# Performance work log

Hardware: AMD Instinct MI355X
Metric: run time of the kernel (lower is better)

## Reference

```python
import jax, jax.numpy as jnp
import numpy as np

PATCH_ORIG = (5, 15, 15)
DWS = [(1, 4, 4), (1, 2, 2), (1, 1, 1)]
STRIDE = [(1, 6, 6), (1, 6, 6), (1, 3, 3)]
EMBED = 32
EPS = 1e-6


def _extract_full_patches(x, shape, stride):
    # x: (N,C,D,H,W) -> (N*P, C, *shape) patches (torch unfold + permute + view)
    N, C = x.shape[:2]
    sp = x.shape[2:]
    nb = tuple((sp[i] - shape[i]) // stride[i] + 1 for i in range(3))
    d = (jnp.arange(nb[0]) * stride[0])[:, None] + jnp.arange(shape[0])[None, :]
    h = (jnp.arange(nb[1]) * stride[1])[:, None] + jnp.arange(shape[1])[None, :]
    w = (jnp.arange(nb[2]) * stride[2])[:, None] + jnp.arange(shape[2])[None, :]
    pat = x[:, :, d[:, None, None, :, None, None],
                  h[None, :, None, None, :, None],
                  w[None, None, :, None, None, :]]
    # (N, C, nb0, nb1, nb2, p0, p1, p2) -> (N*P, C, p0, p1, p2)
    pat = pat.transpose(0, 2, 3, 4, 1, 5, 6, 7).reshape(-1, C, *shape)
    return pat, nb


def _extract_centers(x, stride, offset, nb):
    # 1x1x1 patches at fixed crop offset, limited to nb -> (N*P, C)
    sl = x[:, :, offset[0]::stride[0], offset[1]::stride[1], offset[2]::stride[2]]
    sl = sl[:, :, :nb[0], :nb[1], :nb[2]]
    N, C = sl.shape[:2]
    return sl.transpose(0, 2, 3, 4, 1).reshape(-1, C)


def _maxpool(x, fct):
    # MaxPool3d(kernel=stride=fct) on exactly-divisible dims via reshape trick
    B, C = x.shape[:2]
    p0, p1, p2 = x.shape[2] // fct[0], x.shape[3] // fct[1], x.shape[4] // fct[2]
    x = x.reshape(B, C, p0, fct[0], p1, fct[1], p2, fct[2])
    return x.max(axis=(3, 5, 7))


def _dice(pred, trg):
    # inferno SorensenDiceLoss, channelwise: flatten to (C, -1)
    p = pred.transpose(1, 0, 2, 3, 4).reshape(pred.shape[1], -1)
    t = trg.transpose(1, 0, 2, 3, 4).reshape(trg.shape[1], -1)
    num = (p * t).sum(-1)
    den = jnp.clip((p * p + t * t).sum(-1), EPS, None)
    return (-2.0 * num / den).sum()


def _level_loss(pred, target, W, b, lvl):
    gt = target[:, :1].astype(jnp.float32)           # GT label volume (N,1,D,H,W)
    affs = target[:, 1:].astype(jnp.float32)
    bnd = 1.0 - affs
    bmask = bnd[:, 4:].max(1, keepdims=True) if lvl == 0 else bnd[:, :4].max(1, keepdims=True)
    dws, stride = DWS[lvl], STRIDE[lvl]
    pshape = tuple(p * f for p, f in zip(PATCH_ORIG, dws))
    off = tuple(s // 2 for s in pshape)              # crop offset (rnd crop fixed to 0)

    gt_patches, nb = _extract_full_patches(gt, pshape, stride)   # (P,1,*pshape)
    centers = _extract_centers(gt, stride, off, nb)[:, 0]        # (P,)
    on_bnd = _extract_centers(bmask, stride, off, nb)[:, 0]      # (P,)

    me = (gt_patches != centers[:, None, None, None, None]).astype(jnp.float32)
    ign = (gt_patches == 0).astype(jnp.float32)
    valid = ((centers != 0) & (on_bnd != 1.0)).astype(jnp.float32)

    trg = _maxpool(me, dws)                                      # (P,1,*PATCH_ORIG)
    ign_m = _maxpool(ign, dws) > 0

    emb = _extract_centers(pred, stride, off, nb)                # (P, EMBED)
    pp = jax.nn.sigmoid(emb @ W + b).reshape(-1, 1, *PATCH_ORIG) # patch decoder

    pp = jnp.where(ign_m, 0.0, pp)
    trg = jnp.where(ign_m, 0.0, trg)
    v = valid[:, None, None, None, None]                         # mask == select valid patches for sum-based Dice
    return _dice(pp * v, trg * v)


def setup_inputs() -> dict:
    key = jax.random.key(0)
    ks = jax.random.split(key, 16)
    shapes = [(2, 8, 160, 160), (2, 8, 80, 80), (2, 8, 40, 40)]
    inp = {}
    for lvl, (n, d, hh, ww) in enumerate(shapes):
        inp[f'pred{lvl}'] = jax.random.normal(ks[lvl], (n, EMBED, d, hh, ww), jnp.float32)
        gt = jax.random.randint(ks[3 + lvl], (n, 1, d, hh, ww), 0, 50, jnp.int32)
        affs = jax.random.randint(ks[6 + lvl], (n, 8, d, hh, ww), 0, 2, jnp.int32)
        inp[f'tgt{lvl}'] = jnp.concatenate([gt, affs], axis=1)
        inp[f'W{lvl}'] = 0.1 * jax.random.normal(ks[9 + lvl], (EMBED, int(np.prod(PATCH_ORIG))), jnp.float32)
        inp[f'b{lvl}'] = jnp.zeros((int(np.prod(PATCH_ORIG)),), jnp.float32)
    return inp


def reference(pred0, pred1, pred2, W0, b0, W1, b1, W2, b2, tgt0, tgt1, tgt2):
    loss = _level_loss(pred0, tgt0, W0, b0, 0)
    loss = loss + _level_loss(pred1, tgt1, W1, b1, 1)
    loss = loss + _level_loss(pred2, tgt2, W2, b2, 2)
    return loss
```

## Files before the change

### kernel.cpp

```cpp
#include <hip/hip_runtime.h>
#include <hip/hip_bf16.h>


constexpr int NBATCH = 2;
constexpr int EMB = 32;
constexpr int TGTC = 9;
constexpr int PZ = 5, PY = 15, PX = 15;
constexpr int P = PZ * PY * PX;

constexpr int NBLK0 = NBATCH * 4 * 17 * 17;
constexpr int NBLK1 = NBATCH * 4 * 9 * 9;
constexpr int NBLK2 = NBATCH * 4 * 9 * 9;
constexpr int NBLK_TOT = NBLK0 + NBLK1 + NBLK2;

template <int D, int H, int W,
          int NB0, int NBH, int NBW,
          int SH, int SW,
          int DH, int DWIN,
          int OFFZ, int OFFY, int OFFX,
          int AFFB>
__device__ __forceinline__
void level_body(const int lbid,
                const float* __restrict__ pred,
                const int* __restrict__ tgt,
                const float* __restrict__ Wm,
                const float* __restrict__ bv,
                float* __restrict__ partials)
{
    const int tid = threadIdx.x;

    int k  = lbid % NBW;
    int t1 = lbid / NBW;
    int j  = t1 % NBH;
    int t2 = t1 / NBH;
    int i  = t2 % NB0;
    int b  = t2 / NB0;

    const int HW = H * W;
    const int CH = D * HW;
    const int zc = OFFZ + i;
    const int yc = OFFY + j * SH;
    const int xc = OFFX + k * SW;
    const int cidx = zc * HW + yc * W + xc;

    __shared__ float s_emb[EMB];
    __shared__ int   s_c;
    __shared__ int   s_valid;

    if (tid == 0) {
        const int c = tgt[b * TGTC * CH + cidx];
        bool allaff = true;
        #pragma unroll
        for (int ch = 0; ch < 4; ++ch)
            allaff &= (tgt[(b * TGTC + AFFB + ch) * CH + cidx] != 0);
        s_c = c;
        s_valid = (c != 0) && allaff;
    }
    __syncthreads();

    if (!s_valid) {
        if (tid == 0) {
            partials[2 * lbid]     = 0.0f;
            partials[2 * lbid + 1] = 0.0f;
        }
        return;
    }

    if (tid < EMB)
        s_emb[tid] = pred[(b * EMB + tid) * CH + cidx];
    __syncthreads();

    const int* __restrict__ gtb = tgt + b * TGTC * CH;
    const int c = s_c;

    float num = 0.0f, den = 0.0f;
    for (int o = tid; o < P; o += 256) {
        const int pz = o / (PY * PX);
        const int r  = o - pz * (PY * PX);
        const int py = r / PX;
        const int px = r - py * PX;

        float dot = bv[o];
        #pragma unroll
        for (int e = 0; e < EMB; ++e)
            dot = fmaf(s_emb[e], Wm[e * P + o], dot);
        float pp = 1.0f / (1.0f + expf(-dot));

        const int zb = i + pz;
        const int yb = j * SH + py * DH;
        const int xb = k * SW + px * DWIN;
        bool anyz = false, anyd = false;
        #pragma unroll
        for (int wy = 0; wy < DH; ++wy) {
            #pragma unroll
            for (int wx = 0; wx < DWIN; ++wx) {
                const int g = gtb[zb * HW + (yb + wy) * W + (xb + wx)];
                anyz |= (g == 0);
                anyd |= (g != c);
            }
        }
        float trg = (anyz || !anyd) ? 0.0f : 1.0f;
        if (anyz) pp = 0.0f;

        num = fmaf(pp, trg, num);
        den += pp * pp + trg * trg;
    }

    #pragma unroll
    for (int off = 32; off > 0; off >>= 1) {
        num += __shfl_down(num, off);
        den += __shfl_down(den, off);
    }
    __shared__ float sn[4], sd[4];
    if ((tid & 63) == 0) { sn[tid >> 6] = num; sd[tid >> 6] = den; }
    __syncthreads();
    if (tid == 0) {
        partials[2 * lbid]     = sn[0] + sn[1] + sn[2] + sn[3];
        partials[2 * lbid + 1] = sd[0] + sd[1] + sd[2] + sd[3];
    }
}

__global__ __launch_bounds__(256)
void stage_kernel(const float* __restrict__ pred0, const int* __restrict__ tgt0,
                  const float* __restrict__ W0, const float* __restrict__ b0,
                  const float* __restrict__ pred1, const int* __restrict__ tgt1,
                  const float* __restrict__ W1, const float* __restrict__ b1,
                  const float* __restrict__ pred2, const int* __restrict__ tgt2,
                  const float* __restrict__ W2, const float* __restrict__ b2,
                  float* __restrict__ partials)
{
    const int gb = blockIdx.x;
    if (gb < NBLK0) {
        level_body<8, 160, 160, 4, 17, 17, 6, 6, 4, 4, 2, 30, 30, 5>(
            gb, pred0, tgt0, W0, b0, partials);
    } else if (gb < NBLK0 + NBLK1) {
        level_body<8, 80, 80, 4, 9, 9, 6, 6, 2, 2, 2, 15, 15, 1>(
            gb - NBLK0, pred1, tgt1, W1, b1, partials + 2 * NBLK0);
    } else {
        level_body<8, 40, 40, 4, 9, 9, 3, 3, 1, 1, 2, 7, 7, 1>(
            gb - NBLK0 - NBLK1, pred2, tgt2, W2, b2,
            partials + 2 * (NBLK0 + NBLK1));
    }
}

__global__ __launch_bounds__(256)
void finalize_kernel(const float* __restrict__ partials, float* __restrict__ out)
{
    const int tid = threadIdx.x;
    const int counts[3] = { NBLK0, NBLK1, NBLK2 };
    const int offs[3]   = { 0, NBLK0, NBLK0 + NBLK1 };

    __shared__ float sn[4], sd[4];
    __shared__ float s_loss;
    if (tid == 0) s_loss = 0.0f;
    __syncthreads();

    for (int l = 0; l < 3; ++l) {
        float n = 0.0f, d = 0.0f;
        const float2* p2 = (const float2*)(partials + 2 * offs[l]);
        for (int p = tid; p < counts[l]; p += 256) {
            const float2 v = p2[p];
            n += v.x;
            d += v.y;
        }
        #pragma unroll
        for (int off = 32; off > 0; off >>= 1) {
            n += __shfl_down(n, off);
            d += __shfl_down(d, off);
        }
        if ((tid & 63) == 0) { sn[tid >> 6] = n; sd[tid >> 6] = d; }
        __syncthreads();
        if (tid == 0) {
            const float N_ = sn[0] + sn[1] + sn[2] + sn[3];
            const float D_ = sd[0] + sd[1] + sd[2] + sd[3];
            s_loss += -2.0f * N_ / fmaxf(D_, 1e-6f);
        }
        __syncthreads();
    }
    if (tid == 0) out[0] = s_loss;
}

extern "C" void kernel_launch(void* const* d_in, const int* in_sizes, int n_in,
                              void* d_out, int out_size, void* d_ws, size_t ws_size,
                              hipStream_t stream)
{
    const float* pred0 = (const float*)d_in[0];
    const int*   tgt0  = (const int*)  d_in[1];
    const float* W0    = (const float*)d_in[2];
    const float* b0    = (const float*)d_in[3];
    const float* pred1 = (const float*)d_in[4];
    const int*   tgt1  = (const int*)  d_in[5];
    const float* W1    = (const float*)d_in[6];
    const float* b1    = (const float*)d_in[7];
    const float* pred2 = (const float*)d_in[8];
    const int*   tgt2  = (const int*)  d_in[9];
    const float* W2    = (const float*)d_in[10];
    const float* b2    = (const float*)d_in[11];

    float* out      = (float*)d_out;
    float* partials = (float*)d_ws;

    stage_kernel<<<NBLK_TOT, 256, 0, stream>>>(
        pred0, tgt0, W0, b0, pred1, tgt1, W1, b1, pred2, tgt2, W2, b2,
        partials);
    finalize_kernel<<<1, 256, 0, stream>>>(partials, out);
}
```

Before: 20.49 us.

## Fuse finalize into stage kernel via fixed-point atomics and last-block reduction

Each block now adds its numerator and denominator partial sums as 64-bit fixed-point values to per-level global accumulators with atomics. The last block to finish, found through an atomic counter, computes the loss, so the separate finalize kernel is gone. This removes a kernel launch and the partials round-trip. In exchange it adds a memset of the workspace before the launch, atomic traffic on a few addresses, and fixed-point rounding of the sums.

```diff
diff --git a/kernel.cpp b/kernel.cpp
--- a/kernel.cpp
+++ b/kernel.cpp
@@ -13,6 +13,13 @@
 constexpr int NBLK2 = NBATCH * 4 * 9 * 9;
 constexpr int NBLK_TOT = NBLK0 + NBLK1 + NBLK2;
 
+constexpr double FIX = 4294967296.0;
+
+__device__ __forceinline__ unsigned long long to_fixed(float x)
+{
+    return (unsigned long long)__double2ll_rn((double)x * FIX);
+}
+
 template <int D, int H, int W,
           int NB0, int NBH, int NBW,
           int SH, int SW,
@@ -25,7 +32,8 @@
                 const int* __restrict__ tgt,
                 const float* __restrict__ Wm,
                 const float* __restrict__ bv,
-                float* __restrict__ partials)
+                unsigned long long* __restrict__ accN,
+                unsigned long long* __restrict__ accD)
 {
     const int tid = threadIdx.x;
 
@@ -58,13 +66,8 @@
     }
     __syncthreads();
 
-    if (!s_valid) {
-        if (tid == 0) {
-            partials[2 * lbid]     = 0.0f;
-            partials[2 * lbid + 1] = 0.0f;
-        }
+    if (!s_valid)
         return;
-    }
 
     if (tid < EMB)
         s_emb[tid] = pred[(b * EMB + tid) * CH + cidx];
@@ -115,8 +118,10 @@
     if ((tid & 63) == 0) { sn[tid >> 6] = num; sd[tid >> 6] = den; }
     __syncthreads();
     if (tid == 0) {
-        partials[2 * lbid]     = sn[0] + sn[1] + sn[2] + sn[3];
-        partials[2 * lbid + 1] = sd[0] + sd[1] + sd[2] + sd[3];
+        const float N_ = sn[0] + sn[1] + sn[2] + sn[3];
+        const float D_ = sd[0] + sd[1] + sd[2] + sd[3];
+        atomicAdd(accN, to_fixed(N_));
+        atomicAdd(accD, to_fixed(D_));
     }
 }
 
@@ -127,57 +132,41 @@
                   const float* __restrict__ W1, const float* __restrict__ b1,
                   const float* __restrict__ pred2, const int* __restrict__ tgt2,
                   const float* __restrict__ W2, const float* __restrict__ b2,
-                  float* __restrict__ partials)
+                  unsigned long long* __restrict__ acc,
+                  unsigned int* __restrict__ counter,
+                  float* __restrict__ out)
 {
     const int gb = blockIdx.x;
     if (gb < NBLK0) {
         level_body<8, 160, 160, 4, 17, 17, 6, 6, 4, 4, 2, 30, 30, 5>(
-            gb, pred0, tgt0, W0, b0, partials);
+            gb, pred0, tgt0, W0, b0, acc + 0, acc + 1);
     } else if (gb < NBLK0 + NBLK1) {
         level_body<8, 80, 80, 4, 9, 9, 6, 6, 2, 2, 2, 15, 15, 1>(
-            gb - NBLK0, pred1, tgt1, W1, b1, partials + 2 * NBLK0);
+            gb - NBLK0, pred1, tgt1, W1, b1, acc + 2, acc + 3);
     } else {
         level_body<8, 40, 40, 4, 9, 9, 3, 3, 1, 1, 2, 7, 7, 1>(
-            gb - NBLK0 - NBLK1, pred2, tgt2, W2, b2,
-            partials + 2 * (NBLK0 + NBLK1));
+            gb - NBLK0 - NBLK1, pred2, tgt2, W2, b2, acc + 4, acc + 5);
     }
-}
 
-__global__ __launch_bounds__(256)
-void finalize_kernel(const float* __restrict__ partials, float* __restrict__ out)
-{
-    const int tid = threadIdx.x;
-    const int counts[3] = { NBLK0, NBLK1, NBLK2 };
-    const int offs[3]   = { 0, NBLK0, NBLK0 + NBLK1 };
-
-    __shared__ float sn[4], sd[4];
-    __shared__ float s_loss;
-    if (tid == 0) s_loss = 0.0f;
-    __syncthreads();
-
-    for (int l = 0; l < 3; ++l) {
-        float n = 0.0f, d = 0.0f;
-        const float2* p2 = (const float2*)(partials + 2 * offs[l]);
-        for (int p = tid; p < counts[l]; p += 256) {
-            const float2 v = p2[p];
-            n += v.x;
-            d += v.y;
+    if (threadIdx.x == 0) {
+        __threadfence();
+        const unsigned int old = atomicAdd(counter, 1u);
+        if (old == (unsigned int)(NBLK_TOT - 1)) {
+            __threadfence();
+            double loss = 0.0;
+            #pragma unroll
+            for (int l = 0; l < 3; ++l) {
+                const long long n = (long long)__hip_atomic_load(
+                    acc + 2 * l,     __ATOMIC_RELAXED, __HIP_MEMORY_SCOPE_AGENT);
+                const long long d = (long long)__hip_atomic_load(
+                    acc + 2 * l + 1, __ATOMIC_RELAXED, __HIP_MEMORY_SCOPE_AGENT);
+                const double nd = (double)n / FIX;
+                const double dd = (double)d / FIX;
+                loss += -2.0 * nd / fmax(dd, 1e-6);
+            }
+            out[0] = (float)loss;
         }
-        #pragma unroll
-        for (int off = 32; off > 0; off >>= 1) {
-            n += __shfl_down(n, off);
-            d += __shfl_down(d, off);
-        }
-        if ((tid & 63) == 0) { sn[tid >> 6] = n; sd[tid >> 6] = d; }
-        __syncthreads();
-        if (tid == 0) {
-            const float N_ = sn[0] + sn[1] + sn[2] + sn[3];
-            const float D_ = sd[0] + sd[1] + sd[2] + sd[3];
-            s_loss += -2.0f * N_ / fmaxf(D_, 1e-6f);
-        }
-        __syncthreads();
     }
-    if (tid == 0) out[0] = s_loss;
 }
 
 extern "C" void kernel_launch(void* const* d_in, const int* in_sizes, int n_in,
@@ -197,11 +186,13 @@
     const float* W2    = (const float*)d_in[10];
     const float* b2    = (const float*)d_in[11];
 
-    float* out      = (float*)d_out;
-    float* partials = (float*)d_ws;
+    float* out = (float*)d_out;
+    unsigned long long* acc = (unsigned long long*)d_ws;
+    unsigned int* counter   = (unsigned int*)(acc + 6);
+
+    hipMemsetAsync(d_ws, 0, 64, stream);
 
     stage_kernel<<<NBLK_TOT, 256, 0, stream>>>(
         pred0, tgt0, W0, b0, pred1, tgt1, W1, b1, pred2, tgt2, W2, b2,
-        partials);
-    finalize_kernel<<<1, 256, 0, stream>>>(partials, out);
+        acc, counter, out);
 }
```

New measurement: 77.78 us. 3.8x slower.
